# Performance work log

Measured on AMD Instinct MI355X. Metric: run time of the kernel, lower is better.

The kernel has to match this reference:

```python
import jax, jax.numpy as jnp
import numpy as np

N_NODES = 10000
N_EDGES = 640000
IN_CH = 128
HID = 256
OUT_CH = 10
NUM_GRAPHS = 64
EPS = 0.0  # non-trainable buffer, initial_eps=0


def setup_inputs() -> dict:
    key = jax.random.key(0)
    ks = jax.random.split(key, 12)
    x = jax.random.normal(ks[0], (N_NODES, IN_CH), dtype=jnp.float32)
    edge_index = jax.random.randint(ks[1], (2, N_EDGES), 0, N_NODES, dtype=jnp.int64)
    batch = jnp.sort(jax.random.randint(ks[2], (N_NODES,), 0, NUM_GRAPHS, dtype=jnp.int64))
    edge_weights = jax.random.uniform(ks[3], (N_EDGES,), dtype=jnp.float32)
    def lin(k, fan_in, fan_out):
        bound = 1.0 / np.sqrt(fan_in)
        kw, kb = jax.random.split(k)
        W = jax.random.uniform(kw, (fan_out, fan_in), minval=-bound, maxval=bound, dtype=jnp.float32)
        b = jax.random.uniform(kb, (fan_out,), minval=-bound, maxval=bound, dtype=jnp.float32)
        return W, b
    W1, b1 = lin(ks[4], IN_CH, HID)
    W2, b2 = lin(ks[5], HID, HID)
    W3, b3 = lin(ks[6], HID, HID)
    Wl, bl = lin(ks[7], HID, OUT_CH)
    return {"x": x, "edge_index": edge_index, "batch": batch, "edge_weights": edge_weights,
            "W1": W1, "b1": b1, "W2": W2, "b2": b2, "W3": W3, "b3": b3, "Wl": Wl, "bl": bl}


def _ginw_conv(x, edge_index, edge_weights, W, b):
    # message: edge_weight * x_j (source nodes), aggregated by add at target i
    src, dst = edge_index[0], edge_index[1]
    msg = edge_weights[:, None] * x[src]           # [E, F]
    agg = jax.ops.segment_sum(msg, dst, num_segments=N_NODES)  # [N, F]
    out = agg + (1.0 + EPS) * x
    return out @ W.T + b


def reference(x, edge_index, batch, edge_weights, W1, b1, W2, b2, W3, b3, Wl, bl):
    h = jax.nn.relu(_ginw_conv(x, edge_index, edge_weights, W1, b1))
    h = jax.nn.relu(_ginw_conv(h, edge_index, edge_weights, W2, b2))
    h = jax.nn.relu(_ginw_conv(h, edge_index, edge_weights, W3, b3))
    # global mean pool over graphs
    sums = jax.ops.segment_sum(h, batch, num_segments=NUM_GRAPHS)        # [G, HID]
    cnts = jax.ops.segment_sum(jnp.ones((N_NODES,), h.dtype), batch, num_segments=NUM_GRAPHS)
    pooled = sums / jnp.maximum(cnts, 1.0)[:, None]
    return pooled @ Wl.T + bl
```

## Files before the change

kernel.cpp:

```cpp
#include <hip/hip_runtime.h>
#include <hip/hip_fp16.h>

namespace {
constexpr int NN   = 10000;
constexpr int NE   = 640000;
constexpr int INC  = 128;
constexpr int HIDC = 256;
constexpr int OUTC = 10;
constexpr int NG   = 64;
constexpr int PP   = 8;

constexpr int NB     = 157;
constexpr int G1     = 256;
constexpr int CHUNK1 = NE / G1;
constexpr int CAPB   = 64;
constexpr int LCAP   = 5120;
}

typedef __attribute__((ext_vector_type(8))) short short8;
typedef __attribute__((ext_vector_type(4))) float f32x4;

__device__ __forceinline__ ushort f2bf(float f) {
    uint u = __float_as_uint(f);
    uint r = u + 0x7FFFu + ((u >> 16) & 1u);
    return (ushort)(r >> 16);
}
__device__ __forceinline__ float bf2f(ushort u) {
    return __uint_as_float(((uint)u) << 16);
}
__device__ __forceinline__ float rec_w(uint rec) {
    return __half2float(__ushort_as_half((ushort)(rec & 0xFFFFu)));
}

__global__ __launch_bounds__(256) void partition_kernel(const int* __restrict__ ei,
                                                        const float* __restrict__ ew,
                                                        uint2* __restrict__ stag,
                                                        int* __restrict__ cnts,
                                                        int* __restrict__ cnts_T,
                                                        const float* __restrict__ x,
                                                        ushort* __restrict__ xb) {
    __shared__ int lcnt[NB];
    const int t = threadIdx.x, g = blockIdx.x;
    for (int i = t; i < NB; i += 256) lcnt[i] = 0;
    __syncthreads();
    const int base = g * CHUNK1;
    for (int i = t; i < CHUNK1; i += 256) {
        const int e = base + i;
        const int dst = ei[NE + e];
        const int src = ei[e];
        const ushort hw = __half_as_ushort(__float2half(ew[e]));
        const int bk = dst >> 6;
        const int idx = atomicAdd(&lcnt[bk], 1);
        if (idx < CAPB)
            stag[((size_t)g * NB + bk) * CAPB + idx] =
                make_uint2(((uint)src << 16) | (uint)hw, (uint)dst);
    }
    __syncthreads();
    for (int i = t; i < NB; i += 256) {
        const int c = min(lcnt[i], CAPB);
        cnts[g * NB + i] = c;
        cnts_T[i * G1 + g] = c;
    }
    const int total4 = NN * INC / 4;
    for (int i = g * 256 + t; i < total4; i += G1 * 256) {
        float4 v = ((const float4*)x)[i];
        ushort4 o;
        o.x = f2bf(v.x); o.y = f2bf(v.y); o.z = f2bf(v.z); o.w = f2bf(v.w);
        ((ushort4*)xb)[i] = o;
    }
}

__global__ __launch_bounds__(1024) void place_kernel(const uint2* __restrict__ stag,
                                                     const int* __restrict__ cnts,
                                                     const int* __restrict__ cnts_T,
                                                     int* __restrict__ row_start,
                                                     uint* __restrict__ erec) {
    const int b = blockIdx.x;
    const int t = threadIdx.x;
    __shared__ int part[256];
    __shared__ int foff[G1 + 1];
    __shared__ int h[64];
    __shared__ int curl[64];
    __shared__ uint2 srec[LCAP];

    {
        int s = 0;
        if (t < NB) {
            const int4* r = (const int4*)(cnts_T + (size_t)t * G1);
#pragma unroll 8
            for (int i = 0; i < G1 / 4; i++) {
                int4 v = r[i];
                s += v.x + v.y + v.z + v.w;
            }
        }
        if (t < 256) part[t] = s;
        __syncthreads();
        for (int off = 1; off < 256; off <<= 1) {
            int v = 0;
            if (t < 256 && t >= off) v = part[t - off];
            __syncthreads();
            if (t < 256) part[t] += v;
            __syncthreads();
        }
    }
    const int bs = (b == 0) ? 0 : part[b - 1];
    if (b == 0 && t == 0) row_start[NN] = part[NB - 1];
    __syncthreads();

    {
        int c = 0;
        if (t < 256) c = cnts[t * NB + b];
        if (t < 256) part[t] = c;
        if (t < 64) h[t] = 0;
        __syncthreads();
        for (int off = 1; off < 256; off <<= 1) {
            int v = 0;
            if (t < 256 && t >= off) v = part[t - off];
            __syncthreads();
            if (t < 256) part[t] += v;
            __syncthreads();
        }
        if (t < 256) foff[t] = part[t] - c;
        if (t == 0) foff[G1] = part[255];
        __syncthreads();
    }
    const int Rb = foff[G1];

    for (int r = t; r < Rb; r += 1024) {
        int lo = 0, hi = G1;
        while (hi - lo > 1) { int mid = (lo + hi) >> 1; if (foff[mid] <= r) lo = mid; else hi = mid; }
        uint2 rec = stag[((size_t)lo * NB + b) * CAPB + (r - foff[lo])];
        if (r < LCAP) srec[r] = rec;
        atomicAdd(&h[rec.y & 63], 1);
    }
    __syncthreads();

    {
        const int hv = (t < 64) ? h[t] : 0;
        if (t < 256) part[t] = (t < 64) ? hv : 0;
        __syncthreads();
        for (int off = 1; off < 64; off <<= 1) {
            int v = 0;
            if (t < 256 && t >= off) v = part[t - off];
            __syncthreads();
            if (t < 256) part[t] += v;
            __syncthreads();
        }
        if (t < 64) {
            const int excl = part[t] - hv;
            const int node = b * 64 + t;
            if (node < NN) row_start[node] = bs + excl;
            curl[t] = excl;
        }
        __syncthreads();
    }

    for (int r = t; r < Rb; r += 1024) {
        uint2 rec;
        if (r < LCAP) rec = srec[r];
        else {
            int lo = 0, hi = G1;
            while (hi - lo > 1) { int mid = (lo + hi) >> 1; if (foff[mid] <= r) lo = mid; else hi = mid; }
            rec = stag[((size_t)lo * NB + b) * CAPB + (r - foff[lo])];
        }
        const int pos = bs + atomicAdd(&curl[rec.y & 63], 1);
        erec[pos] = rec.x;
    }
}

template <int F>
__global__ __launch_bounds__(256) void gather_bf16_kernel(const int* __restrict__ row_start,
                                                          const uint* __restrict__ erec,
                                                          const ushort* __restrict__ x,
                                                          ushort* __restrict__ out) {
    constexpr int VEC = F / 64;
    constexpr int U = 12;
    const int n = blockIdx.x * 4 + (threadIdx.x >> 6);
    const int lane = threadIdx.x & 63;
    if (n >= NN) return;
    const int beg = row_start[n];
    const int end = row_start[n + 1];
    const size_t loff = (size_t)lane * VEC;

    float acc[VEC];
    {
        ushort v[VEC];
        if (VEC == 4) *(ushort4*)v = *(const ushort4*)(x + (size_t)n * F + loff);
        else          *(ushort2*)v = *(const ushort2*)(x + (size_t)n * F + loff);
#pragma unroll
        for (int i = 0; i < VEC; i++) acc[i] = bf2f(v[i]);
    }

    int e = beg;
    for (; e + U <= end; e += U) {
        uint rec[U];
#pragma unroll
        for (int u = 0; u < U; u++) rec[u] = erec[e + u];
        ushort v[U][VEC];
#pragma unroll
        for (int u = 0; u < U; u++) {
            const ushort* r = x + (size_t)(rec[u] >> 16) * F + loff;
            if (VEC == 4) *(ushort4*)v[u] = *(const ushort4*)r;
            else          *(ushort2*)v[u] = *(const ushort2*)r;
        }
#pragma unroll
        for (int u = 0; u < U; u++) {
            const float w = rec_w(rec[u]);
#pragma unroll
            for (int i = 0; i < VEC; i++) acc[i] += w * bf2f(v[u][i]);
        }
    }
    for (; e < end; e++) {
        uint rec = erec[e];
        const float w = rec_w(rec);
        ushort v[VEC];
        const ushort* r = x + (size_t)(rec >> 16) * F + loff;
        if (VEC == 4) *(ushort4*)v = *(const ushort4*)r;
        else          *(ushort2*)v = *(const ushort2*)r;
#pragma unroll
        for (int i = 0; i < VEC; i++) acc[i] += w * bf2f(v[i]);
    }

    ushort o[VEC];
#pragma unroll
    for (int i = 0; i < VEC; i++) o[i] = f2bf(acc[i]);
    if (VEC == 4) *(ushort4*)(out + (size_t)n * F + loff) = *(ushort4*)o;
    else          *(ushort2*)(out + (size_t)n * F + loff) = *(ushort2*)o;
}

__global__ __launch_bounds__(256) void gather_bf16_half_kernel(const int* __restrict__ row_start,
                                                               const uint* __restrict__ erec,
                                                               const ushort* __restrict__ x,
                                                               ushort* __restrict__ out) {
    constexpr int U = 16;
    const int n = blockIdx.x * 4 + (threadIdx.x >> 6);
    const int lane = threadIdx.x & 63;
    if (n >= NN) return;
    const int beg = row_start[n];
    const int end = row_start[n + 1];
    const size_t loff = (size_t)blockIdx.y * 128 + lane * 2;

    float acc[2];
    {
        ushort2 v = *(const ushort2*)(x + (size_t)n * HIDC + loff);
        acc[0] = bf2f(v.x);
        acc[1] = bf2f(v.y);
    }

    int e = beg;
    for (; e + U <= end; e += U) {
        uint rec[U];
#pragma unroll
        for (int u = 0; u < U; u++) rec[u] = erec[e + u];
        ushort2 v[U];
#pragma unroll
        for (int u = 0; u < U; u++)
            v[u] = *(const ushort2*)(x + (size_t)(rec[u] >> 16) * HIDC + loff);
#pragma unroll
        for (int u = 0; u < U; u++) {
            const float w = rec_w(rec[u]);
            acc[0] += w * bf2f(v[u].x);
            acc[1] += w * bf2f(v[u].y);
        }
    }
    for (; e < end; e++) {
        uint rec = erec[e];
        const float w = rec_w(rec);
        ushort2 v = *(const ushort2*)(x + (size_t)(rec >> 16) * HIDC + loff);
        acc[0] += w * bf2f(v.x);
        acc[1] += w * bf2f(v.y);
    }

    ushort2 o;
    o.x = f2bf(acc[0]);
    o.y = f2bf(acc[1]);
    *(ushort2*)(out + (size_t)n * HIDC + loff) = o;
}

template <int K>
__global__ __launch_bounds__(256) void mfma_gemm_kernel(const ushort* __restrict__ A,
                                                        const float* __restrict__ W,
                                                        const float* __restrict__ bias,
                                                        ushort* __restrict__ C, int M) {
    constexpr int LDW = K + 8;
    __shared__ ushort Ws[64 * LDW];
    const int tid = threadIdx.x;
    const int bm = blockIdx.x * 128;
    const int bn = blockIdx.y * 64;

    constexpr int CPR = K / 4;
    for (int idx = tid; idx < 64 * CPR; idx += 256) {
        int r = idx / CPR, c = idx % CPR;
        float4 v = *(const float4*)(W + (size_t)(bn + r) * K + c * 4);
        ushort4 o;
        o.x = f2bf(v.x); o.y = f2bf(v.y); o.z = f2bf(v.z); o.w = f2bf(v.w);
        *(ushort4*)(&Ws[r * LDW + c * 4]) = o;
    }
    __syncthreads();

    const int wave = tid >> 6;
    const int lane = tid & 63;
    const int lrow = lane & 15;
    const int lq   = lane >> 4;
    const int m0 = bm + wave * 32;

    f32x4 acc[2][4] = {};
    const int r0 = min(m0 + lrow, M - 1);
    const int r1 = min(m0 + 16 + lrow, M - 1);

    for (int k0 = 0; k0 < K; k0 += 32) {
        const int kk = k0 + lq * 8;
        short8 a0 = *(const short8*)(A + (size_t)r0 * K + kk);
        short8 a1 = *(const short8*)(A + (size_t)r1 * K + kk);
        short8 b[4];
#pragma unroll
        for (int j = 0; j < 4; j++)
            b[j] = *(const short8*)(&Ws[(j * 16 + lrow) * LDW + kk]);
#pragma unroll
        for (int j = 0; j < 4; j++) {
            acc[0][j] = __builtin_amdgcn_mfma_f32_16x16x32_bf16(a0, b[j], acc[0][j], 0, 0, 0);
            acc[1][j] = __builtin_amdgcn_mfma_f32_16x16x32_bf16(a1, b[j], acc[1][j], 0, 0, 0);
        }
    }

#pragma unroll
    for (int sub = 0; sub < 2; sub++) {
#pragma unroll
        for (int j = 0; j < 4; j++) {
            const int gn = bn + j * 16 + lrow;
            const float bv = bias[gn];
#pragma unroll
            for (int i = 0; i < 4; i++) {
                const int gm = m0 + sub * 16 + lq * 4 + i;
                if (gm < M) {
                    float v = acc[sub][j][i] + bv;
                    v = fmaxf(v, 0.0f);
                    C[(size_t)gm * HIDC + gn] = f2bf(v);
                }
            }
        }
    }
}

__device__ __forceinline__ int lower_bound_batch(const int* __restrict__ batch, int val) {
    int lo = 0, hi = NN;
    while (lo < hi) {
        int mid = (lo + hi) >> 1;
        if (batch[mid] < val) lo = mid + 1;
        else hi = mid;
    }
    return lo;
}

__global__ __launch_bounds__(256) void pool_partial_kernel(const ushort* __restrict__ h,
                                                           const int* __restrict__ batch,
                                                           float* __restrict__ partials) {
    const int g = blockIdx.x;
    const int p = blockIdx.y;
    const int c = threadIdx.x;
    const int lo = lower_bound_batch(batch, g);
    const int hi = lower_bound_batch(batch, g + 1);
    const int cnt = hi - lo;
    const int chunk = (cnt + PP - 1) / PP;
    const int n0 = lo + p * chunk;
    const int n1 = min(hi, n0 + chunk);
    float sum = 0.0f;
    for (int n = n0; n < n1; n++) sum += bf2f(h[(size_t)n * HIDC + c]);
    partials[((size_t)g * PP + p) * HIDC + c] = sum;
}

__global__ __launch_bounds__(256) void head_kernel(const float* __restrict__ partials,
                                                   const int* __restrict__ batch,
                                                   const float* __restrict__ Wl,
                                                   const float* __restrict__ bl,
                                                   float* __restrict__ out) {
    __shared__ float s[HIDC];
    const int g = blockIdx.x;
    const int c = threadIdx.x;
    const int lo = lower_bound_batch(batch, g);
    const int hi = lower_bound_batch(batch, g + 1);
    const float inv = 1.0f / fmaxf((float)(hi - lo), 1.0f);
    float sum = 0.0f;
#pragma unroll
    for (int p = 0; p < PP; p++) sum += partials[((size_t)g * PP + p) * HIDC + c];
    s[c] = sum * inv;
    __syncthreads();
    if (c < OUTC) {
        float acc = bl[c];
        for (int k = 0; k < HIDC; k++) acc += s[k] * Wl[(size_t)c * HIDC + k];
        out[(size_t)g * OUTC + c] = acc;
    }
}

extern "C" void kernel_launch(void* const* d_in, const int* in_sizes, int n_in,
                              void* d_out, int out_size, void* d_ws, size_t ws_size,
                              hipStream_t stream) {
    const float* x     = (const float*)d_in[0];
    const int*   ei    = (const int*)d_in[1];
    const int*   batch = (const int*)d_in[2];
    const float* ew    = (const float*)d_in[3];
    const float* W1    = (const float*)d_in[4];
    const float* b1    = (const float*)d_in[5];
    const float* W2    = (const float*)d_in[6];
    const float* b2    = (const float*)d_in[7];
    const float* W3    = (const float*)d_in[8];
    const float* b3    = (const float*)d_in[9];
    const float* Wl    = (const float*)d_in[10];
    const float* bl    = (const float*)d_in[11];

    char* p = (char*)d_ws;
    uint2*  stag   = (uint2*)p;  p += (size_t)G1 * NB * CAPB * 8;
    ushort* xb     = (ushort*)p; p += (size_t)NN * INC * 2;
    ushort* agg128 = (ushort*)p; p += (size_t)NN * INC * 2;
    ushort* agg256 = (ushort*)p; p += (size_t)NN * HIDC * 2;
    ushort* h      = (ushort*)p; p += (size_t)NN * HIDC * 2;
    uint*   erec   = (uint*)p;   p += (size_t)NE * 4;
    float*  partials = (float*)p; p += (size_t)NG * PP * HIDC * 4;
    int*    cnts   = (int*)p;    p += (size_t)G1 * NB * 4;
    int*    cnts_T = (int*)p;    p += (size_t)NB * G1 * 4;
    int*    row_start = (int*)p; p += 40016;

    partition_kernel<<<G1, 256, 0, stream>>>(ei, ew, stag, cnts, cnts_T, x, xb);
    place_kernel<<<NB, 1024, 0, stream>>>(stag, cnts, cnts_T, row_start, erec);

    const int gather_grid = (NN + 3) / 4;
    dim3 gemm_grid((NN + 127) / 128, HIDC / 64);

    gather_bf16_kernel<INC><<<gather_grid, 256, 0, stream>>>(row_start, erec, xb, agg128);
    mfma_gemm_kernel<INC><<<gemm_grid, 256, 0, stream>>>(agg128, W1, b1, h, NN);

    gather_bf16_half_kernel<<<dim3(gather_grid, 2), 256, 0, stream>>>(row_start, erec, h, agg256);
    mfma_gemm_kernel<HIDC><<<gemm_grid, 256, 0, stream>>>(agg256, W2, b2, h, NN);

    gather_bf16_half_kernel<<<dim3(gather_grid, 2), 256, 0, stream>>>(row_start, erec, h, agg256);
    mfma_gemm_kernel<HIDC><<<gemm_grid, 256, 0, stream>>>(agg256, W3, b3, h, NN);

    pool_partial_kernel<<<dim3(NG, PP), 256, 0, stream>>>(h, batch, partials);
    head_kernel<<<NG, 256, 0, stream>>>(partials, batch, Wl, bl, (float*)d_out);
}
```

Measured before the change: 242.3 us.

## Preconvert weights to bf16, predicate gather tails, split half-gathers into launches

Converts W1/W2/W3 to bf16 once in the partition kernel, so each GEMM block copies ready bf16 weights into shared memory instead of converting fp32 per block. The gather kernels replace the scalar remainder loop with a predicated, fully unrolled 16-wide loop (unroll raised from 12 to 16 for the 128-channel gather). Each 256-channel gather is now two separate launches, one per half, instead of a 2D grid. This cuts redundant weight conversion and tail-loop latency, but adds two kernel launches and wasted loads on padded edge slots.

```diff
diff --git a/kernel.cpp b/kernel.cpp
--- a/kernel.cpp
+++ b/kernel.cpp
@@ -38,7 +38,13 @@
                                                         int* __restrict__ cnts,
                                                         int* __restrict__ cnts_T,
                                                         const float* __restrict__ x,
-                                                        ushort* __restrict__ xb) {
+                                                        ushort* __restrict__ xb,
+                                                        const float* __restrict__ W1,
+                                                        ushort* __restrict__ w1b,
+                                                        const float* __restrict__ W2,
+                                                        ushort* __restrict__ w2b,
+                                                        const float* __restrict__ W3,
+                                                        ushort* __restrict__ w3b) {
     __shared__ int lcnt[NB];
     const int t = threadIdx.x, g = blockIdx.x;
     for (int i = t; i < NB; i += 256) lcnt[i] = 0;
@@ -61,12 +67,33 @@
         cnts[g * NB + i] = c;
         cnts_T[i * G1 + g] = c;
     }
-    const int total4 = NN * INC / 4;
-    for (int i = g * 256 + t; i < total4; i += G1 * 256) {
-        float4 v = ((const float4*)x)[i];
-        ushort4 o;
-        o.x = f2bf(v.x); o.y = f2bf(v.y); o.z = f2bf(v.z); o.w = f2bf(v.w);
-        ((ushort4*)xb)[i] = o;
+    const int gt = g * 256 + t, gs = G1 * 256;
+    {
+        const int n4 = NN * INC / 4;
+        for (int i = gt; i < n4; i += gs) {
+            float4 v = ((const float4*)x)[i];
+            ushort4 o; o.x = f2bf(v.x); o.y = f2bf(v.y); o.z = f2bf(v.z); o.w = f2bf(v.w);
+            ((ushort4*)xb)[i] = o;
+        }
+    }
+    {
+        const int n4 = HIDC * INC / 4;
+        for (int i = gt; i < n4; i += gs) {
+            float4 v = ((const float4*)W1)[i];
+            ushort4 o; o.x = f2bf(v.x); o.y = f2bf(v.y); o.z = f2bf(v.z); o.w = f2bf(v.w);
+            ((ushort4*)w1b)[i] = o;
+        }
+    }
+    {
+        const int n4 = HIDC * HIDC / 4;
+        for (int i = gt; i < n4; i += gs) {
+            float4 v = ((const float4*)W2)[i];
+            ushort4 o; o.x = f2bf(v.x); o.y = f2bf(v.y); o.z = f2bf(v.z); o.w = f2bf(v.w);
+            ((ushort4*)w2b)[i] = o;
+            float4 v3 = ((const float4*)W3)[i];
+            ushort4 o3; o3.x = f2bf(v3.x); o3.y = f2bf(v3.y); o3.z = f2bf(v3.z); o3.w = f2bf(v3.w);
+            ((ushort4*)w3b)[i] = o3;
+        }
     }
 }
 
@@ -174,7 +201,7 @@
                                                           const ushort* __restrict__ x,
                                                           ushort* __restrict__ out) {
     constexpr int VEC = F / 64;
-    constexpr int U = 12;
+    constexpr int U = 16;
     const int n = blockIdx.x * 4 + (threadIdx.x >> 6);
     const int lane = threadIdx.x & 63;
     if (n >= NN) return;
@@ -191,11 +218,16 @@
         for (int i = 0; i < VEC; i++) acc[i] = bf2f(v[i]);
     }
 
-    int e = beg;
-    for (; e + U <= end; e += U) {
+    for (int e = beg; e < end; e += U) {
         uint rec[U];
-#pragma unroll
-        for (int u = 0; u < U; u++) rec[u] = erec[e + u];
+        float w[U];
+#pragma unroll
+        for (int u = 0; u < U; u++) {
+            const int idx = e + u;
+            const bool ok = idx < end;
+            rec[u] = erec[ok ? idx : (end - 1)];
+            w[u] = ok ? rec_w(rec[u]) : 0.0f;
+        }
         ushort v[U][VEC];
 #pragma unroll
         for (int u = 0; u < U; u++) {
@@ -205,20 +237,9 @@
         }
 #pragma unroll
         for (int u = 0; u < U; u++) {
-            const float w = rec_w(rec[u]);
-#pragma unroll
-            for (int i = 0; i < VEC; i++) acc[i] += w * bf2f(v[u][i]);
-        }
-    }
-    for (; e < end; e++) {
-        uint rec = erec[e];
-        const float w = rec_w(rec);
-        ushort v[VEC];
-        const ushort* r = x + (size_t)(rec >> 16) * F + loff;
-        if (VEC == 4) *(ushort4*)v = *(const ushort4*)r;
-        else          *(ushort2*)v = *(const ushort2*)r;
-#pragma unroll
-        for (int i = 0; i < VEC; i++) acc[i] += w * bf2f(v[i]);
+#pragma unroll
+            for (int i = 0; i < VEC; i++) acc[i] += w[u] * bf2f(v[u][i]);
+        }
     }
 
     ushort o[VEC];
@@ -231,55 +252,53 @@
 __global__ __launch_bounds__(256) void gather_bf16_half_kernel(const int* __restrict__ row_start,
                                                                const uint* __restrict__ erec,
                                                                const ushort* __restrict__ x,
-                                                               ushort* __restrict__ out) {
+                                                               ushort* __restrict__ out,
+                                                               int half) {
     constexpr int U = 16;
     const int n = blockIdx.x * 4 + (threadIdx.x >> 6);
     const int lane = threadIdx.x & 63;
     if (n >= NN) return;
     const int beg = row_start[n];
     const int end = row_start[n + 1];
-    const size_t loff = (size_t)blockIdx.y * 128 + lane * 2;
-
-    float acc[2];
+    const size_t loff = (size_t)half * 128 + lane * 2;
+
+    float acc0, acc1;
     {
         ushort2 v = *(const ushort2*)(x + (size_t)n * HIDC + loff);
-        acc[0] = bf2f(v.x);
-        acc[1] = bf2f(v.y);
-    }
-
-    int e = beg;
-    for (; e + U <= end; e += U) {
+        acc0 = bf2f(v.x);
+        acc1 = bf2f(v.y);
+    }
+
+    for (int e = beg; e < end; e += U) {
         uint rec[U];
-#pragma unroll
-        for (int u = 0; u < U; u++) rec[u] = erec[e + u];
+        float w[U];
+#pragma unroll
+        for (int u = 0; u < U; u++) {
+            const int idx = e + u;
+            const bool ok = idx < end;
+            rec[u] = erec[ok ? idx : (end - 1)];
+            w[u] = ok ? rec_w(rec[u]) : 0.0f;
+        }
         ushort2 v[U];
 #pragma unroll
         for (int u = 0; u < U; u++)
             v[u] = *(const ushort2*)(x + (size_t)(rec[u] >> 16) * HIDC + loff);
 #pragma unroll
         for (int u = 0; u < U; u++) {
-            const float w = rec_w(rec[u]);
-            acc[0] += w * bf2f(v[u].x);
-            acc[1] += w * bf2f(v[u].y);
-        }
-    }
-    for (; e < end; e++) {
-        uint rec = erec[e];
-        const float w = rec_w(rec);
-        ushort2 v = *(const ushort2*)(x + (size_t)(rec >> 16) * HIDC + loff);
-        acc[0] += w * bf2f(v.x);
-        acc[1] += w * bf2f(v.y);
+            acc0 += w[u] * bf2f(v[u].x);
+            acc1 += w[u] * bf2f(v[u].y);
+        }
     }
 
     ushort2 o;
-    o.x = f2bf(acc[0]);
-    o.y = f2bf(acc[1]);
+    o.x = f2bf(acc0);
+    o.y = f2bf(acc1);
     *(ushort2*)(out + (size_t)n * HIDC + loff) = o;
 }
 
 template <int K>
 __global__ __launch_bounds__(256) void mfma_gemm_kernel(const ushort* __restrict__ A,
-                                                        const float* __restrict__ W,
+                                                        const ushort* __restrict__ Wb,
                                                         const float* __restrict__ bias,
                                                         ushort* __restrict__ C, int M) {
     constexpr int LDW = K + 8;
@@ -288,13 +307,11 @@
     const int bm = blockIdx.x * 128;
     const int bn = blockIdx.y * 64;
 
-    constexpr int CPR = K / 4;
+    constexpr int CPR = K / 8;
     for (int idx = tid; idx < 64 * CPR; idx += 256) {
         int r = idx / CPR, c = idx % CPR;
-        float4 v = *(const float4*)(W + (size_t)(bn + r) * K + c * 4);
-        ushort4 o;
-        o.x = f2bf(v.x); o.y = f2bf(v.y); o.z = f2bf(v.z); o.w = f2bf(v.w);
-        *(ushort4*)(&Ws[r * LDW + c * 4]) = o;
+        uint4 v = *(const uint4*)(Wb + (size_t)(bn + r) * K + c * 8);
+        *(uint4*)(&Ws[r * LDW + c * 8]) = v;
     }
     __syncthreads();
 
@@ -414,26 +431,32 @@
     ushort* agg128 = (ushort*)p; p += (size_t)NN * INC * 2;
     ushort* agg256 = (ushort*)p; p += (size_t)NN * HIDC * 2;
     ushort* h      = (ushort*)p; p += (size_t)NN * HIDC * 2;
+    ushort* w1b    = (ushort*)p; p += (size_t)HIDC * INC * 2;
+    ushort* w2b    = (ushort*)p; p += (size_t)HIDC * HIDC * 2;
+    ushort* w3b    = (ushort*)p; p += (size_t)HIDC * HIDC * 2;
     uint*   erec   = (uint*)p;   p += (size_t)NE * 4;
     float*  partials = (float*)p; p += (size_t)NG * PP * HIDC * 4;
     int*    cnts   = (int*)p;    p += (size_t)G1 * NB * 4;
     int*    cnts_T = (int*)p;    p += (size_t)NB * G1 * 4;
     int*    row_start = (int*)p; p += 40016;
 
-    partition_kernel<<<G1, 256, 0, stream>>>(ei, ew, stag, cnts, cnts_T, x, xb);
+    partition_kernel<<<G1, 256, 0, stream>>>(ei, ew, stag, cnts, cnts_T, x, xb,
+                                             W1, w1b, W2, w2b, W3, w3b);
     place_kernel<<<NB, 1024, 0, stream>>>(stag, cnts, cnts_T, row_start, erec);
 
     const int gather_grid = (NN + 3) / 4;
     dim3 gemm_grid((NN + 127) / 128, HIDC / 64);
 
     gather_bf16_kernel<INC><<<gather_grid, 256, 0, stream>>>(row_start, erec, xb, agg128);
-    mfma_gemm_kernel<INC><<<gemm_grid, 256, 0, stream>>>(agg128, W1, b1, h, NN);
-
-    gather_bf16_half_kernel<<<dim3(gather_grid, 2), 256, 0, stream>>>(row_start, erec, h, agg256);
-    mfma_gemm_kernel<HIDC><<<gemm_grid, 256, 0, stream>>>(agg256, W2, b2, h, NN);
-
-    gather_bf16_half_kernel<<<dim3(gather_grid, 2), 256, 0, stream>>>(row_start, erec, h, agg256);
-    mfma_gemm_kernel<HIDC><<<gemm_grid, 256, 0, stream>>>(agg256, W3, b3, h, NN);
+    mfma_gemm_kernel<INC><<<gemm_grid, 256, 0, stream>>>(agg128, w1b, b1, h, NN);
+
+    gather_bf16_half_kernel<<<gather_grid, 256, 0, stream>>>(row_start, erec, h, agg256, 0);
+    gather_bf16_half_kernel<<<gather_grid, 256, 0, stream>>>(row_start, erec, h, agg256, 1);
+    mfma_gemm_kernel<HIDC><<<gemm_grid, 256, 0, stream>>>(agg256, w2b, b2, h, NN);
+
+    gather_bf16_half_kernel<<<gather_grid, 256, 0, stream>>>(row_start, erec, h, agg256, 0);
+    gather_bf16_half_kernel<<<gather_grid, 256, 0, stream>>>(row_start, erec, h, agg256, 1);
+    mfma_gemm_kernel<HIDC><<<gemm_grid, 256, 0, stream>>>(agg256, w3b, b3, h, NN);
 
     pool_partial_kernel<<<dim3(NG, PP), 256, 0, stream>>>(h, batch, partials);
     head_kernel<<<NG, 256, 0, stream>>>(partials, batch, Wl, bl, (float*)d_out);
```

New measurement: 260.2 us. 1.07x slower.
